# Performance work log

Hardware: AMD Instinct MI355X
Metric: run time of the kernel (lower is better)

Reference implementation:

```python
import jax, jax.numpy as jnp
import numpy as np

D_MODEL = 1024
N_HEADS = 16
D_HEAD = D_MODEL // N_HEADS
B, T = 2, 2048


def setup_inputs() -> dict:
    key = jax.random.key(0)
    ks = jax.random.split(key, 6)
    scale = 1.0 / np.sqrt(D_MODEL)
    x = jax.random.normal(ks[0], (B, T, D_MODEL), dtype=jnp.float32)
    mask = jax.random.randint(ks[1], (1, 1, T, T), 0, 2, dtype=jnp.int32)
    Wqkv = jax.random.normal(ks[2], (D_MODEL, 3 * D_MODEL), dtype=jnp.float32) * scale
    bqkv = jnp.zeros((3 * D_MODEL,), dtype=jnp.float32)
    Wproj = jax.random.normal(ks[3], (D_MODEL, D_MODEL), dtype=jnp.float32) * scale
    bproj = jnp.zeros((D_MODEL,), dtype=jnp.float32)
    return {"x": x, "mask": mask, "Wqkv": Wqkv, "bqkv": bqkv,
            "Wproj": Wproj, "bproj": bproj}


def reference(x, mask, Wqkv, bqkv, Wproj, bproj):
    Bx, Tx, C = x.shape
    qkv = x @ Wqkv + bqkv                      # [B,T,3C]
    q, k, v = jnp.split(qkv, 3, axis=-1)       # each [B,T,C]

    def heads(t):  # [B,T,C] -> [B,H,T,dh]
        return t.reshape(Bx, Tx, N_HEADS, D_HEAD).transpose(0, 2, 1, 3)

    q, k, v = heads(q), heads(k), heads(v)
    att = jnp.einsum('bhqd,bhkd->bhqk', q, k) / jnp.sqrt(jnp.float32(D_HEAD))
    att = jnp.where(mask == 1, -jnp.inf, att)
    att = jax.nn.softmax(att, axis=-1)
    out = jnp.einsum('bhqk,bhkd->bhqd', att, v)  # [B,H,T,dh]
    out = out.transpose(0, 2, 1, 3).reshape(Bx, Tx, C)
    return out @ Wproj + bproj
```

## Files before the change

kernel.cpp:

```cpp
#include <hip/hip_runtime.h>
#include <hip/hip_bf16.h>

#define T_DIM 2048
#define C_DIM 1024
#define NHEAD 16
#define DHEAD 64

typedef __attribute__((ext_vector_type(8))) short s16x8;
typedef __attribute__((ext_vector_type(4))) float f32x4;
typedef __attribute__((ext_vector_type(4))) unsigned short u16x4;

static __device__ __forceinline__ unsigned short f2bfu(float f){
  __hip_bfloat16 h = __float2bfloat16(f);
  unsigned short u;
  __builtin_memcpy(&u, &h, 2);
  return u;
}

static __device__ __forceinline__ f32x4 MFMA16(s16x8 a, s16x8 b, f32x4 c){
  return __builtin_amdgcn_mfma_f32_16x16x32_bf16(a, b, c, 0, 0, 0);
}

__global__ __launch_bounds__(256) void cvt_bf16_kernel(const float* __restrict__ in,
                                                       unsigned short* __restrict__ out, int n4){
  int i = blockIdx.x*256 + threadIdx.x;
  if (i < n4){
    float4 v = reinterpret_cast<const float4*>(in)[i];
    u16x4 o;
    o.x = f2bfu(v.x); o.y = f2bfu(v.y); o.z = f2bfu(v.z); o.w = f2bfu(v.w);
    reinterpret_cast<u16x4*>(out)[i] = o;
  }
}

__global__ __launch_bounds__(256) void transpose_cvt_kernel(const float* __restrict__ src,
                                                            unsigned short* __restrict__ dst,
                                                            int K, int N){
  __shared__ unsigned short tile[64][65];
  int n0 = blockIdx.x*64, k0 = blockIdx.y*64;
  int tid = threadIdx.x;
  #pragma unroll
  for (int i=0;i<16;i++){
    int e = i*256 + tid; int r = e>>6, c = e&63;
    tile[r][c] = f2bfu(src[(size_t)(k0+r)*N + n0 + c]);
  }
  __syncthreads();
  #pragma unroll
  for (int i=0;i<16;i++){
    int e = i*256 + tid; int r = e>>6, c = e&63;
    dst[(size_t)(n0+r)*K + k0 + c] = tile[c][r];
  }
}

__global__ __launch_bounds__(256) void mask_bits_kernel(const int* __restrict__ m,
                                                        unsigned int* __restrict__ bits){
  int i = blockIdx.x*256 + threadIdx.x;
  unsigned long long b = __ballot(m[i] == 1);
  int lane = threadIdx.x & 63;
  if (lane == 0)  bits[i>>5] = (unsigned int)b;
  if (lane == 32) bits[i>>5] = (unsigned int)(b>>32);
}

__global__ __launch_bounds__(256) void transpose_v_kernel(const unsigned short* __restrict__ v,
                                                          unsigned short* __restrict__ vt){
  __shared__ unsigned short tile[64][65];
  int bh = blockIdx.y;
  int t0 = blockIdx.x*64;
  const unsigned short* src = v + (size_t)bh*T_DIM*DHEAD;
  unsigned short* dst = vt + (size_t)bh*T_DIM*DHEAD;
  int tid = threadIdx.x;
  #pragma unroll
  for (int i=0;i<16;i++){
    int e = i*256+tid; int r = e>>6, c = e&63;
    tile[r][c] = src[(size_t)(t0+r)*DHEAD + c];
  }
  __syncthreads();
  #pragma unroll
  for (int i=0;i<16;i++){
    int e = i*256+tid; int r = e>>6, c = e&63;
    dst[(size_t)r*T_DIM + t0 + c] = tile[c][r];
  }
}

template<int MODE>
__global__ __launch_bounds__(256) void gemm_kernel(const unsigned short* __restrict__ A,
    const unsigned short* __restrict__ Bt, const float* __restrict__ bias,
    unsigned short* __restrict__ qo, unsigned short* __restrict__ ko,
    unsigned short* __restrict__ vo, float* __restrict__ out)
{
  const int K = 1024;
  __shared__ __align__(16) unsigned short As[128][72];
  __shared__ __align__(16) unsigned short Bs[128][72];
  int tid = threadIdx.x;
  int lane = tid & 63, wave = tid >> 6;
  int m0 = blockIdx.y*128, n0 = blockIdx.x*128;
  int wm = (wave>>1)*64, wn = (wave&1)*64;
  int lr = lane & 15, lg = lane >> 4;
  f32x4 acc[4][4];
  #pragma unroll
  for (int i=0;i<4;i++){
    #pragma unroll
    for (int j=0;j<4;j++){
      #pragma unroll
      for (int r=0;r<4;r++) acc[i][j][r] = 0.f;
    }
  }
  for (int kt=0; kt<K; kt+=64){
    #pragma unroll
    for (int it=0; it<4; it++){
      int t = it*256 + tid;
      int r = t>>3, ch = (t&7)*8;
      *reinterpret_cast<s16x8*>(&As[r][ch]) =
          *reinterpret_cast<const s16x8*>(A + (size_t)(m0+r)*K + kt + ch);
      *reinterpret_cast<s16x8*>(&Bs[r][ch]) =
          *reinterpret_cast<const s16x8*>(Bt + (size_t)(n0+r)*K + kt + ch);
    }
    __syncthreads();
    #pragma unroll
    for (int kk=0; kk<2; kk++){
      s16x8 av[4], bv[4];
      #pragma unroll
      for (int i=0;i<4;i++){
        av[i] = *reinterpret_cast<const s16x8*>(&As[wm + i*16 + lr][kk*32 + lg*8]);
        bv[i] = *reinterpret_cast<const s16x8*>(&Bs[wn + i*16 + lr][kk*32 + lg*8]);
      }
      #pragma unroll
      for (int i=0;i<4;i++){
        #pragma unroll
        for (int j=0;j<4;j++)
          acc[i][j] = MFMA16(av[i], bv[j], acc[i][j]);
      }
    }
    __syncthreads();
  }
  #pragma unroll
  for (int j=0;j<4;j++){
    int n = n0 + wn + j*16 + lr;
    float bvl = bias[n];
    #pragma unroll
    for (int i=0;i<4;i++){
      #pragma unroll
      for (int r=0;r<4;r++){
        int m = m0 + wm + i*16 + lg*4 + r;
        float val = acc[i][j][r] + bvl;
        if (MODE == 0){
          int which = n >> 10, c = n & 1023;
          int h = c >> 6, d = c & 63;
          int b = m >> 11, t = m & 2047;
          size_t idx = ((size_t)((b*NHEAD + h)*T_DIM + t))*DHEAD + d;
          unsigned short us = f2bfu(val);
          if (which == 0) qo[idx] = us;
          else if (which == 1) ko[idx] = us;
          else vo[idx] = us;
        } else {
          out[(size_t)m*C_DIM + n] = val;
        }
      }
    }
  }
}

__global__ __launch_bounds__(256) void attn_kernel(const unsigned short* __restrict__ q,
    const unsigned short* __restrict__ k, const unsigned short* __restrict__ vt,
    const unsigned int* __restrict__ mbits, unsigned short* __restrict__ aout)
{
  __shared__ __align__(16) unsigned short Ks[64][72];
  __shared__ __align__(16) unsigned short Vs[64][72];
  __shared__ __align__(16) unsigned short Ps[4][16][72];
  int bh = blockIdx.y;
  int q0 = blockIdx.x*64;
  int tid = threadIdx.x, lane = tid&63, wave = tid>>6;
  int lr = lane&15, lg = lane>>4;
  const unsigned short* qp = q  + (size_t)bh*T_DIM*DHEAD;
  const unsigned short* kp = k  + (size_t)bh*T_DIM*DHEAD;
  const unsigned short* vp = vt + (size_t)bh*T_DIM*DHEAD;
  int qw = q0 + wave*16;
  s16x8 qf[2];
  #pragma unroll
  for (int kk=0;kk<2;kk++)
    qf[kk] = *reinterpret_cast<const s16x8*>(qp + (size_t)(qw+lr)*DHEAD + kk*32 + lg*8);
  f32x4 o[4];
  #pragma unroll
  for (int cb=0;cb<4;cb++){
    #pragma unroll
    for (int r=0;r<4;r++) o[cb][r]=0.f;
  }
  float mrow[4], lrow[4];
  #pragma unroll
  for (int r=0;r<4;r++){ mrow[r] = -1e30f; lrow[r]=0.f; }
  int qbase = qw + lg*4;

  for (int k0=0; k0<T_DIM; k0+=64){
    #pragma unroll
    for (int it=0; it<2; it++){
      int t = it*256 + tid;
      int r = t>>3, ch = (t&7)*8;
      *reinterpret_cast<s16x8*>(&Ks[r][ch]) =
          *reinterpret_cast<const s16x8*>(kp + (size_t)(k0+r)*DHEAD + ch);
      *reinterpret_cast<s16x8*>(&Vs[r][ch]) =
          *reinterpret_cast<const s16x8*>(vp + (size_t)r*T_DIM + k0 + ch);
    }
    __syncthreads();
    f32x4 s[4];
    #pragma unroll
    for (int cb=0;cb<4;cb++){
      f32x4 a;
      #pragma unroll
      for (int r=0;r<4;r++) a[r]=0.f;
      #pragma unroll
      for (int kk=0;kk<2;kk++){
        s16x8 kf = *reinterpret_cast<const s16x8*>(&Ks[cb*16 + lr][kk*32 + lg*8]);
        a = MFMA16(qf[kk], kf, a);
      }
      s[cb] = a;
    }
    #pragma unroll
    for (int cb=0;cb<4;cb++){
      int kc = k0 + cb*16 + lr;
      int w = kc >> 5, bit = kc & 31;
      #pragma unroll
      for (int r=0;r<4;r++){
        unsigned mw = mbits[(size_t)(qbase + r)*(T_DIM/32) + w];
        float val = s[cb][r]*0.125f;
        s[cb][r] = ((mw>>bit)&1u) ? -1e30f : val;
      }
    }
    #pragma unroll
    for (int r=0;r<4;r++){
      float mx = fmaxf(fmaxf(s[0][r], s[1][r]), fmaxf(s[2][r], s[3][r]));
      mx = fmaxf(mx, __shfl_xor(mx, 1));
      mx = fmaxf(mx, __shfl_xor(mx, 2));
      mx = fmaxf(mx, __shfl_xor(mx, 4));
      mx = fmaxf(mx, __shfl_xor(mx, 8));
      float mnew = fmaxf(mrow[r], mx);
      float corr = __expf(mrow[r] - mnew);
      mrow[r] = mnew;
      float rs = 0.f;
      #pragma unroll
      for (int cb=0;cb<4;cb++){
        float p = __expf(s[cb][r] - mnew);
        s[cb][r] = p;
        rs += p;
      }
      rs += __shfl_xor(rs, 1);
      rs += __shfl_xor(rs, 2);
      rs += __shfl_xor(rs, 4);
      rs += __shfl_xor(rs, 8);
      lrow[r] = lrow[r]*corr + rs;
      #pragma unroll
      for (int cb=0;cb<4;cb++) o[cb][r] *= corr;
    }
    #pragma unroll
    for (int cb=0;cb<4;cb++){
      #pragma unroll
      for (int r=0;r<4;r++)
        Ps[wave][lg*4 + r][cb*16 + lr] = f2bfu(s[cb][r]);
    }
    s16x8 pf[2];
    #pragma unroll
    for (int kk=0;kk<2;kk++)
      pf[kk] = *reinterpret_cast<const s16x8*>(&Ps[wave][lr][kk*32 + lg*8]);
    #pragma unroll
    for (int cb=0;cb<4;cb++){
      #pragma unroll
      for (int kk=0;kk<2;kk++){
        s16x8 vf = *reinterpret_cast<const s16x8*>(&Vs[cb*16 + lr][kk*32 + lg*8]);
        o[cb] = MFMA16(pf[kk], vf, o[cb]);
      }
    }
    __syncthreads();
  }
  int b = bh >> 4, h = bh & 15;
  #pragma unroll
  for (int r=0;r<4;r++){
    float inv = lrow[r] > 0.f ? 1.f/lrow[r] : 0.f;
    int row = b*T_DIM + qbase + r;
    #pragma unroll
    for (int cb=0;cb<4;cb++){
      int d = cb*16 + lr;
      aout[(size_t)row*C_DIM + h*DHEAD + d] = f2bfu(o[cb][r]*inv);
    }
  }
}

extern "C" void kernel_launch(void* const* d_in, const int* in_sizes, int n_in,
                              void* d_out, int out_size, void* d_ws, size_t ws_size,
                              hipStream_t stream){
  const float* x     = (const float*)d_in[0];
  const int*   mask  = (const int*)d_in[1];
  const float* Wqkv  = (const float*)d_in[2];
  const float* bqkv  = (const float*)d_in[3];
  const float* Wproj = (const float*)d_in[4];
  const float* bproj = (const float*)d_in[5];
  float* out = (float*)d_out;
  char* ws = (char*)d_ws;
  const size_t MB = (size_t)1<<20;
  unsigned short* xb     = (unsigned short*)(ws + 0*MB);
  unsigned short* wqkvT  = (unsigned short*)(ws + 8*MB);
  unsigned short* wprojT = (unsigned short*)(ws + 14*MB);
  unsigned int*   mbits  = (unsigned int*)(ws + 16*MB);
  unsigned short* qb     = (unsigned short*)(ws + 17*MB);
  unsigned short* kb     = (unsigned short*)(ws + 25*MB);
  unsigned short* vb     = (unsigned short*)(ws + 33*MB);
  unsigned short* vtb    = (unsigned short*)(ws + 41*MB);
  unsigned short* aout   = xb;

  cvt_bf16_kernel<<<dim3(4096), dim3(256), 0, stream>>>(x, xb, (2*2048*1024)/4);
  transpose_cvt_kernel<<<dim3(48,16), dim3(256), 0, stream>>>(Wqkv, wqkvT, 1024, 3072);
  transpose_cvt_kernel<<<dim3(16,16), dim3(256), 0, stream>>>(Wproj, wprojT, 1024, 1024);
  mask_bits_kernel<<<dim3((2048*2048)/256), dim3(256), 0, stream>>>(mask, mbits);
  gemm_kernel<0><<<dim3(24,32), dim3(256), 0, stream>>>(xb, wqkvT, bqkv, qb, kb, vb, nullptr);
  transpose_v_kernel<<<dim3(32,32), dim3(256), 0, stream>>>(vb, vtb);
  attn_kernel<<<dim3(32,32), dim3(256), 0, stream>>>(qb, kb, vtb, mbits, aout);
  gemm_kernel<1><<<dim3(8,32), dim3(256), 0, stream>>>(aout, wprojT, bproj, nullptr, nullptr, nullptr, out);
}
```

Baseline: 293.4 us.

## Compute transposed S tile so each lane owns one query row in softmax

Swaps the MFMA operands so the score tile comes out transposed, with each lane holding 16 key scores for a single query row. The per-row max and sum then need only two cross-lane shuffles instead of four per row for four rows, and the mask is read as two 32-bit words per lane instead of sixteen scattered loads. The P tile is stored to shared memory as packed 4-element vectors. The cost is extra shuffles to redistribute the correction and normalisation factors back to the output layout.

```diff
diff --git a/kernel.cpp b/kernel.cpp
--- a/kernel.cpp
+++ b/kernel.cpp
@@ -7,6 +7,7 @@
 #define DHEAD 64
 
 typedef __attribute__((ext_vector_type(8))) short s16x8;
+typedef __attribute__((ext_vector_type(4))) short s16x4;
 typedef __attribute__((ext_vector_type(4))) float f32x4;
 typedef __attribute__((ext_vector_type(4))) unsigned short u16x4;
 
@@ -184,10 +185,8 @@
     #pragma unroll
     for (int r=0;r<4;r++) o[cb][r]=0.f;
   }
-  float mrow[4], lrow[4];
-  #pragma unroll
-  for (int r=0;r<4;r++){ mrow[r] = -1e30f; lrow[r]=0.f; }
-  int qbase = qw + lg*4;
+  float m = -1e30f, l = 0.f;
+  const unsigned int* mptr = mbits + (size_t)(qw + lr)*(T_DIM/32);
 
   for (int k0=0; k0<T_DIM; k0+=64){
     #pragma unroll
@@ -200,7 +199,7 @@
           *reinterpret_cast<const s16x8*>(vp + (size_t)r*T_DIM + k0 + ch);
     }
     __syncthreads();
-    f32x4 s[4];
+    f32x4 st[4];
     #pragma unroll
     for (int cb=0;cb<4;cb++){
       f32x4 a;
@@ -209,51 +208,60 @@
       #pragma unroll
       for (int kk=0;kk<2;kk++){
         s16x8 kf = *reinterpret_cast<const s16x8*>(&Ks[cb*16 + lr][kk*32 + lg*8]);
-        a = MFMA16(qf[kk], kf, a);
-      }
-      s[cb] = a;
-    }
-    #pragma unroll
-    for (int cb=0;cb<4;cb++){
-      int kc = k0 + cb*16 + lr;
-      int w = kc >> 5, bit = kc & 31;
+        a = MFMA16(kf, qf[kk], a);
+      }
+      st[cb] = a;
+    }
+    unsigned mw0 = mptr[(k0>>5)];
+    unsigned mw1 = mptr[(k0>>5)+1];
+    #pragma unroll
+    for (int cb=0;cb<4;cb++){
+      unsigned msel = (cb<2) ? mw0 : mw1;
+      unsigned ms = msel >> ((cb&1)*16 + lg*4);
       #pragma unroll
       for (int r=0;r<4;r++){
-        unsigned mw = mbits[(size_t)(qbase + r)*(T_DIM/32) + w];
-        float val = s[cb][r]*0.125f;
-        s[cb][r] = ((mw>>bit)&1u) ? -1e30f : val;
-      }
-    }
-    #pragma unroll
-    for (int r=0;r<4;r++){
-      float mx = fmaxf(fmaxf(s[0][r], s[1][r]), fmaxf(s[2][r], s[3][r]));
-      mx = fmaxf(mx, __shfl_xor(mx, 1));
-      mx = fmaxf(mx, __shfl_xor(mx, 2));
-      mx = fmaxf(mx, __shfl_xor(mx, 4));
-      mx = fmaxf(mx, __shfl_xor(mx, 8));
-      float mnew = fmaxf(mrow[r], mx);
-      float corr = __expf(mrow[r] - mnew);
-      mrow[r] = mnew;
-      float rs = 0.f;
-      #pragma unroll
-      for (int cb=0;cb<4;cb++){
-        float p = __expf(s[cb][r] - mnew);
-        s[cb][r] = p;
+        float val = st[cb][r]*0.125f;
+        st[cb][r] = ((ms>>r)&1u) ? -1e30f : val;
+      }
+    }
+    float pmax = st[0][0];
+    #pragma unroll
+    for (int cb=0;cb<4;cb++){
+      #pragma unroll
+      for (int r=0;r<4;r++) pmax = fmaxf(pmax, st[cb][r]);
+    }
+    pmax = fmaxf(pmax, __shfl_xor(pmax, 16));
+    pmax = fmaxf(pmax, __shfl_xor(pmax, 32));
+    float mnew = fmaxf(m, pmax);
+    float corr = __expf(m - mnew);
+    m = mnew;
+    float rs = 0.f;
+    #pragma unroll
+    for (int cb=0;cb<4;cb++){
+      #pragma unroll
+      for (int r=0;r<4;r++){
+        float p = __expf(st[cb][r] - mnew);
+        st[cb][r] = p;
         rs += p;
       }
-      rs += __shfl_xor(rs, 1);
-      rs += __shfl_xor(rs, 2);
-      rs += __shfl_xor(rs, 4);
-      rs += __shfl_xor(rs, 8);
-      lrow[r] = lrow[r]*corr + rs;
-      #pragma unroll
-      for (int cb=0;cb<4;cb++) o[cb][r] *= corr;
-    }
-    #pragma unroll
-    for (int cb=0;cb<4;cb++){
-      #pragma unroll
-      for (int r=0;r<4;r++)
-        Ps[wave][lg*4 + r][cb*16 + lr] = f2bfu(s[cb][r]);
+    }
+    rs += __shfl_xor(rs, 16);
+    rs += __shfl_xor(rs, 32);
+    l = l*corr + rs;
+    float corrO[4];
+    #pragma unroll
+    for (int r=0;r<4;r++) corrO[r] = __shfl(corr, lg*4 + r);
+    #pragma unroll
+    for (int cb=0;cb<4;cb++){
+      #pragma unroll
+      for (int r=0;r<4;r++) o[cb][r] *= corrO[r];
+    }
+    #pragma unroll
+    for (int cb=0;cb<4;cb++){
+      s16x4 pk;
+      #pragma unroll
+      for (int r=0;r<4;r++) pk[r] = (short)f2bfu(st[cb][r]);
+      *reinterpret_cast<s16x4*>(&Ps[wave][lr][cb*16 + lg*4]) = pk;
     }
     s16x8 pf[2];
     #pragma unroll
@@ -270,14 +278,15 @@
     __syncthreads();
   }
   int b = bh >> 4, h = bh & 15;
+  float inv = l > 0.f ? 1.f/l : 0.f;
   #pragma unroll
   for (int r=0;r<4;r++){
-    float inv = lrow[r] > 0.f ? 1.f/lrow[r] : 0.f;
-    int row = b*T_DIM + qbase + r;
+    float invO = __shfl(inv, lg*4 + r);
+    int row = b*T_DIM + qw + lg*4 + r;
     #pragma unroll
     for (int cb=0;cb<4;cb++){
       int d = cb*16 + lr;
-      aout[(size_t)row*C_DIM + h*DHEAD + d] = f2bfu(o[cb][r]*inv);
+      aout[(size_t)row*C_DIM + h*DHEAD + d] = f2bfu(o[cb][r]*invO);
     }
   }
 }
```

Result: faster. 256.7 us (-12.5%).
